# Kernel optimization log

Hardware: AMD Instinct MI355X
Metric: run time of the kernel (lower is better)

## Reference

```python
import jax, jax.numpy as jnp
import numpy as np
import math

N_HEADS = 32
N_REP = 4
N_KV = N_HEADS // N_REP
HEAD_DIM = 128
MAX_SEQ = 4096
BATCH = 8
Q_LEN = 1


def setup_inputs() -> dict:
    key = jax.random.key(0)
    ks = jax.random.split(key, 7)
    input_pos = jax.random.randint(ks[0], (Q_LEN,), 0, MAX_SEQ, dtype=jnp.int32)
    q = jax.random.normal(ks[1], (N_HEADS, BATCH, Q_LEN, HEAD_DIM), dtype=jnp.float32)
    k = jax.random.normal(ks[2], (N_KV, BATCH, Q_LEN, HEAD_DIM), dtype=jnp.float32)
    v = jax.random.normal(ks[3], (N_KV, BATCH, Q_LEN, HEAD_DIM), dtype=jnp.float32)
    k_cache = jax.random.normal(ks[4], (N_KV, BATCH, MAX_SEQ, HEAD_DIM), dtype=jnp.float32)
    v_cache = jax.random.normal(ks[5], (N_KV, BATCH, MAX_SEQ, HEAD_DIM), dtype=jnp.float32)
    mask = jax.random.normal(ks[6], (MAX_SEQ, MAX_SEQ), dtype=jnp.float32)
    return {"input_pos": input_pos, "q": q, "k": k, "v": v,
            "k_cache": k_cache, "v_cache": v_cache, "mask": mask}


def reference(input_pos, q, k, v, k_cache, v_cache, mask):
    # KV cache update (index_put_ at positions input_pos along seq axis)
    kc = k_cache.at[:, :, input_pos, :].set(k)   # [G, B, S, D]
    vc = v_cache.at[:, :, input_pos, :].set(v)   # [G, B, S, D]
    scale = 1.0 / math.sqrt(HEAD_DIM)
    # group query heads by kv head: head i uses kv group i // n_rep
    qg = q.reshape(N_KV, N_REP, BATCH, Q_LEN, HEAD_DIM)
    scores = jnp.einsum('grbqd,gbsd->grbqs', qg, kc) * scale
    scores = scores + mask[input_pos]            # [Q, S] broadcast
    probs = jax.nn.softmax(scores, axis=-1)
    out = jnp.einsum('grbqs,gbsd->grbqd', probs, vc)  # [G, R, B, Q, D]
    # torch.cat over heads (i = g*n_rep + r) on last dim -> [B, Q, H*D]
    out = out.transpose(2, 3, 0, 1, 4).reshape(BATCH, Q_LEN, N_HEADS * HEAD_DIM)
    return out
```

## Files before the change

### kernel.cpp

```cpp
#include <hip/hip_runtime.h>
#include <math.h>

#define NKV    8
#define NREP   4
#define NH     32
#define BATCH  8
#define D      128
#define SEQ    4096
#define CHUNKS 16
#define CS     256
#define PSTRIDE 130

__global__ __launch_bounds__(256, 4) void attn_partial(
    const int*   __restrict__ input_pos,
    const float* __restrict__ q,
    const float* __restrict__ knew,
    const float* __restrict__ vnew,
    const float* __restrict__ kcache,
    const float* __restrict__ vcache,
    const float* __restrict__ mask,
    float*       __restrict__ ws)
{
    const int pair = blockIdx.x;
    const int c    = blockIdx.y;
    const int g    = pair >> 3;
    const int b    = pair & 7;
    const int t    = threadIdx.x;
    const int w    = t >> 6;
    const int lane = t & 63;
    const int p4   = lane >> 4;
    const int l16  = lane & 15;
    const int half = lane >> 5;
    const int l32  = lane & 31;
    const int pos  = input_pos[0];

    __shared__ float sc[NREP][CS];
    __shared__ float ml[NREP][2];
    __shared__ float opart[4][NREP][D];

    const float  scale  = 0.08838834764831845f;
    const size_t kvbase = (size_t)(g * BATCH + b) * SEQ * D;
    const float* kbase  = kcache + kvbase;
    const float* vbase  = vcache + kvbase;
    const float* mrow   = mask + (size_t)pos * SEQ;
    const float* knewr  = knew + (size_t)(g * BATCH + b) * D;
    const float* vnewr  = vnew + (size_t)(g * BATCH + b) * D;
    const int    s0     = c * CS;
    const int    rowbase = w * 64;

    float4 qv[NREP][2];
    #pragma unroll
    for (int r = 0; r < NREP; ++r) {
        const float4* qr = (const float4*)(q + ((size_t)(g * NREP + r) * BATCH + b) * D
                                           + l16 * 8);
        qv[r][0] = qr[0];
        qv[r][1] = qr[1];
    }

    #pragma unroll
    for (int i = 0; i < 16; ++i) {
        const int sl = rowbase + i * 4 + p4;
        const int s  = s0 + sl;
        const float* krow = (s == pos) ? knewr : (kbase + (size_t)s * D);
        const float4* k4  = (const float4*)(krow + l16 * 8);
        const float4 k0 = k4[0], k1 = k4[1];
        float acc[NREP];
        #pragma unroll
        for (int r = 0; r < NREP; ++r) {
            float a;
            a = k0.x * qv[r][0].x;
            a = fmaf(k0.y, qv[r][0].y, a);
            a = fmaf(k0.z, qv[r][0].z, a);
            a = fmaf(k0.w, qv[r][0].w, a);
            a = fmaf(k1.x, qv[r][1].x, a);
            a = fmaf(k1.y, qv[r][1].y, a);
            a = fmaf(k1.z, qv[r][1].z, a);
            a = fmaf(k1.w, qv[r][1].w, a);
            acc[r] = a;
        }
        #pragma unroll
        for (int off = 1; off < 16; off <<= 1) {
            #pragma unroll
            for (int r = 0; r < NREP; ++r)
                acc[r] += __shfl_xor(acc[r], off);
        }
        if (l16 == 0) {
            const float mval = mrow[s];
            #pragma unroll
            for (int r = 0; r < NREP; ++r)
                sc[r][sl] = fmaf(acc[r], scale, mval);
        }
    }
    __syncthreads();

    {
        const int r = w;
        float v0 = sc[r][lane];
        float v1 = sc[r][lane + 64];
        float v2 = sc[r][lane + 128];
        float v3 = sc[r][lane + 192];
        float m  = fmaxf(fmaxf(v0, v1), fmaxf(v2, v3));
        #pragma unroll
        for (int off = 1; off < 64; off <<= 1)
            m = fmaxf(m, __shfl_xor(m, off));
        float e0 = __expf(v0 - m);
        float e1 = __expf(v1 - m);
        float e2 = __expf(v2 - m);
        float e3 = __expf(v3 - m);
        sc[r][lane]       = e0;
        sc[r][lane + 64]  = e1;
        sc[r][lane + 128] = e2;
        sc[r][lane + 192] = e3;
        float l = (e0 + e1) + (e2 + e3);
        #pragma unroll
        for (int off = 1; off < 64; off <<= 1)
            l += __shfl_xor(l, off);
        if (lane == 0) { ml[r][0] = m; ml[r][1] = l; }
    }
    __syncthreads();

    float4 oacc[NREP];
    #pragma unroll
    for (int r = 0; r < NREP; ++r) oacc[r] = make_float4(0.f, 0.f, 0.f, 0.f);

    #pragma unroll
    for (int it = 0; it < 32; ++it) {
        const int sl = rowbase + it * 2 + half;
        const int s  = s0 + sl;
        const float* vrow = (s == pos) ? vnewr : (vbase + (size_t)s * D);
        const float4 v4 = *(const float4*)(vrow + l32 * 4);
        #pragma unroll
        for (int r = 0; r < NREP; ++r) {
            const float pr = sc[r][sl];
            oacc[r].x = fmaf(pr, v4.x, oacc[r].x);
            oacc[r].y = fmaf(pr, v4.y, oacc[r].y);
            oacc[r].z = fmaf(pr, v4.z, oacc[r].z);
            oacc[r].w = fmaf(pr, v4.w, oacc[r].w);
        }
    }
    #pragma unroll
    for (int r = 0; r < NREP; ++r) {
        oacc[r].x += __shfl_xor(oacc[r].x, 32);
        oacc[r].y += __shfl_xor(oacc[r].y, 32);
        oacc[r].z += __shfl_xor(oacc[r].z, 32);
        oacc[r].w += __shfl_xor(oacc[r].w, 32);
    }
    if (half == 0) {
        #pragma unroll
        for (int r = 0; r < NREP; ++r)
            *(float4*)&opart[w][r][l32 * 4] = oacc[r];
    }
    __syncthreads();

    #pragma unroll
    for (int ii = 0; ii < 2; ++ii) {
        int idx = t + ii * 256;
        int r   = idx >> 7;
        int d   = idx & 127;
        float sum = opart[0][r][d] + opart[1][r][d]
                  + opart[2][r][d] + opart[3][r][d];
        size_t base = (((size_t)pair * CHUNKS + c) * NREP + r) * PSTRIDE;
        ws[base + d] = sum;
        if (d == 0) { ws[base + 128] = ml[r][0]; ws[base + 129] = ml[r][1]; }
    }
}

__global__ __launch_bounds__(128) void attn_reduce(
    const float* __restrict__ ws, float* __restrict__ out)
{
    const int idx  = blockIdx.x;
    const int pair = idx >> 2;
    const int r    = idx & 3;
    const int g    = pair >> 3;
    const int b    = pair & 7;
    const int d    = threadIdx.x;

    float mv[CHUNKS], lv[CHUNKS];
    float M = -INFINITY;
    #pragma unroll
    for (int c = 0; c < CHUNKS; ++c) {
        size_t base = (((size_t)pair * CHUNKS + c) * NREP + r) * PSTRIDE;
        float2 t = *(const float2*)&ws[base + 128];
        mv[c] = t.x; lv[c] = t.y;
        M = fmaxf(M, t.x);
    }
    float acc = 0.f, L = 0.f;
    #pragma unroll
    for (int c = 0; c < CHUNKS; ++c) {
        size_t base = (((size_t)pair * CHUNKS + c) * NREP + r) * PSTRIDE;
        float wgt = __expf(mv[c] - M);
        acc += ws[base + d] * wgt;
        L   += lv[c] * wgt;
    }
    int h = g * NREP + r;
    out[(size_t)b * (NH * D) + h * D + d] = acc / L;
}

__global__ __launch_bounds__(256) void attn_full(
    const int*   __restrict__ input_pos,
    const float* __restrict__ q,
    const float* __restrict__ knew,
    const float* __restrict__ vnew,
    const float* __restrict__ kcache,
    const float* __restrict__ vcache,
    const float* __restrict__ mask,
    float*       __restrict__ out)
{
    const int idx = blockIdx.x;
    const int h   = idx >> 3;
    const int b   = idx & 7;
    const int g   = h >> 2;
    const int t   = threadIdx.x;
    const int wave = t >> 6, lane = t & 63, half = lane >> 5, l32 = lane & 31;
    const int pos = input_pos[0];

    __shared__ float sc[SEQ];
    __shared__ float wred[4];
    __shared__ float oacc[2][D];

    const size_t kvbase = (size_t)(g * BATCH + b) * SEQ * D;
    const float* kbase  = kcache + kvbase;
    const float* vbase  = vcache + kvbase;
    const float* mrow   = mask + (size_t)pos * SEQ;
    const float* knewr  = knew + (size_t)(g * BATCH + b) * D;
    const float* vnewr  = vnew + (size_t)(g * BATCH + b) * D;
    const float  scale  = 0.08838834764831845f;

    float4 qv = ((const float4*)(q + (size_t)(h * BATCH + b) * D))[l32];

    for (int p = 0; p < SEQ / 8; ++p) {
        int s = p * 8 + wave * 2 + half;
        const float4* krow = (s == pos) ? (const float4*)knewr
                                        : (const float4*)(kbase + (size_t)s * D);
        float4 kv = krow[l32];
        float acc = qv.x * kv.x + qv.y * kv.y + qv.z * kv.z + qv.w * kv.w;
        #pragma unroll
        for (int off = 1; off < 32; off <<= 1)
            acc += __shfl_xor(acc, off);
        if (l32 == 0) sc[s] = acc * scale + mrow[s];
    }
    __syncthreads();

    float m = -INFINITY;
    for (int s = t; s < SEQ; s += 256) m = fmaxf(m, sc[s]);
    #pragma unroll
    for (int off = 1; off < 64; off <<= 1) m = fmaxf(m, __shfl_xor(m, off));
    if (lane == 0) wred[wave] = m;
    __syncthreads();
    m = fmaxf(fmaxf(wred[0], wred[1]), fmaxf(wred[2], wred[3]));
    __syncthreads();

    float l = 0.f;
    for (int s = t; s < SEQ; s += 256) { float e = __expf(sc[s] - m); sc[s] = e; l += e; }
    #pragma unroll
    for (int off = 1; off < 64; off <<= 1) l += __shfl_xor(l, off);
    __syncthreads();
    if (lane == 0) wred[wave] = l;
    __syncthreads();
    float L = wred[0] + wred[1] + wred[2] + wred[3];

    {
        int hf = t >> 7, d = t & 127;
        float acc = 0.f;
        for (int s = hf * (SEQ / 2); s < (hf + 1) * (SEQ / 2); ++s) {
            const float* vrow = (s == pos) ? vnewr : (vbase + (size_t)s * D);
            acc += sc[s] * vrow[d];
        }
        oacc[hf][d] = acc;
    }
    __syncthreads();
    if (t < D) out[(size_t)b * (NH * D) + h * D + t] = (oacc[0][t] + oacc[1][t]) / L;
}

extern "C" void kernel_launch(void* const* d_in, const int* in_sizes, int n_in,
                              void* d_out, int out_size, void* d_ws, size_t ws_size,
                              hipStream_t stream) {
    const int*   input_pos = (const int*)  d_in[0];
    const float* q         = (const float*)d_in[1];
    const float* k         = (const float*)d_in[2];
    const float* v         = (const float*)d_in[3];
    const float* kcache    = (const float*)d_in[4];
    const float* vcache    = (const float*)d_in[5];
    const float* mask      = (const float*)d_in[6];
    float* out = (float*)d_out;

    const size_t need = (size_t)64 * CHUNKS * NREP * PSTRIDE * sizeof(float);
    if (ws_size >= need) {
        dim3 g1(64, CHUNKS);
        attn_partial<<<g1, 256, 0, stream>>>(input_pos, q, k, v, kcache, vcache, mask,
                                             (float*)d_ws);
        attn_reduce<<<256, 128, 0, stream>>>((const float*)d_ws, out);
    } else {
        attn_full<<<256, 256, 0, stream>>>(input_pos, q, k, v, kcache, vcache, mask, out);
    }
}
```

Before: 54.56 us.

## Make each wavefront an independent 64-row split to drop block barriers

Each wavefront now owns its own 64-position strip and computes its own softmax max and sum. It writes its partial output and statistics straight to the workspace, which removes all three __syncthreads and the cross-wave shared-memory reduction. In exchange the workspace holds four times as many partials (64 strips instead of 16 chunks). The reduce kernel now loops over a runtime chunk count without unrolling, so it reads more data and may stall more on loads.

```diff
diff --git a/kernel.cpp b/kernel.cpp
--- a/kernel.cpp
+++ b/kernel.cpp
@@ -7,8 +7,7 @@
 #define BATCH  8
 #define D      128
 #define SEQ    4096
-#define CHUNKS 16
-#define CS     256
+#define STRIPS 64
 #define PSTRIDE 130
 
 __global__ __launch_bounds__(256, 4) void attn_partial(
@@ -22,7 +21,6 @@
     float*       __restrict__ ws)
 {
     const int pair = blockIdx.x;
-    const int c    = blockIdx.y;
     const int g    = pair >> 3;
     const int b    = pair & 7;
     const int t    = threadIdx.x;
@@ -33,10 +31,11 @@
     const int half = lane >> 5;
     const int l32  = lane & 31;
     const int pos  = input_pos[0];
-
-    __shared__ float sc[NREP][CS];
-    __shared__ float ml[NREP][2];
-    __shared__ float opart[4][NREP][D];
+    const int strip = blockIdx.y * 4 + w;
+    const int s0    = strip * 64;
+
+    __shared__ float sc_all[4][NREP][STRIPS];
+    float (*scw)[STRIPS] = sc_all[w];
 
     const float  scale  = 0.08838834764831845f;
     const size_t kvbase = (size_t)(g * BATCH + b) * SEQ * D;
@@ -45,8 +44,6 @@
     const float* mrow   = mask + (size_t)pos * SEQ;
     const float* knewr  = knew + (size_t)(g * BATCH + b) * D;
     const float* vnewr  = vnew + (size_t)(g * BATCH + b) * D;
-    const int    s0     = c * CS;
-    const int    rowbase = w * 64;
 
     float4 qv[NREP][2];
     #pragma unroll
@@ -59,7 +56,7 @@
 
     #pragma unroll
     for (int i = 0; i < 16; ++i) {
-        const int sl = rowbase + i * 4 + p4;
+        const int sl = i * 4 + p4;
         const int s  = s0 + sl;
         const float* krow = (s == pos) ? knewr : (kbase + (size_t)s * D);
         const float4* k4  = (const float4*)(krow + l16 * 8);
@@ -88,36 +85,36 @@
             const float mval = mrow[s];
             #pragma unroll
             for (int r = 0; r < NREP; ++r)
-                sc[r][sl] = fmaf(acc[r], scale, mval);
-        }
-    }
-    __syncthreads();
-
+                scw[r][sl] = fmaf(acc[r], scale, mval);
+        }
+    }
+
+    const int rep  = lane >> 4;
+    const int row0 = lane & 15;
+    float mO, lO;
     {
-        const int r = w;
-        float v0 = sc[r][lane];
-        float v1 = sc[r][lane + 64];
-        float v2 = sc[r][lane + 128];
-        float v3 = sc[r][lane + 192];
+        float v0 = scw[rep][row0];
+        float v1 = scw[rep][row0 + 16];
+        float v2 = scw[rep][row0 + 32];
+        float v3 = scw[rep][row0 + 48];
         float m  = fmaxf(fmaxf(v0, v1), fmaxf(v2, v3));
         #pragma unroll
-        for (int off = 1; off < 64; off <<= 1)
+        for (int off = 1; off < 16; off <<= 1)
             m = fmaxf(m, __shfl_xor(m, off));
         float e0 = __expf(v0 - m);
         float e1 = __expf(v1 - m);
         float e2 = __expf(v2 - m);
         float e3 = __expf(v3 - m);
-        sc[r][lane]       = e0;
-        sc[r][lane + 64]  = e1;
-        sc[r][lane + 128] = e2;
-        sc[r][lane + 192] = e3;
+        scw[rep][row0]      = e0;
+        scw[rep][row0 + 16] = e1;
+        scw[rep][row0 + 32] = e2;
+        scw[rep][row0 + 48] = e3;
         float l = (e0 + e1) + (e2 + e3);
         #pragma unroll
-        for (int off = 1; off < 64; off <<= 1)
+        for (int off = 1; off < 16; off <<= 1)
             l += __shfl_xor(l, off);
-        if (lane == 0) { ml[r][0] = m; ml[r][1] = l; }
-    }
-    __syncthreads();
+        mO = m; lO = l;
+    }
 
     float4 oacc[NREP];
     #pragma unroll
@@ -125,13 +122,13 @@
 
     #pragma unroll
     for (int it = 0; it < 32; ++it) {
-        const int sl = rowbase + it * 2 + half;
+        const int sl = it * 2 + half;
         const int s  = s0 + sl;
         const float* vrow = (s == pos) ? vnewr : (vbase + (size_t)s * D);
         const float4 v4 = *(const float4*)(vrow + l32 * 4);
         #pragma unroll
         for (int r = 0; r < NREP; ++r) {
-            const float pr = sc[r][sl];
+            const float pr = scw[r][sl];
             oacc[r].x = fmaf(pr, v4.x, oacc[r].x);
             oacc[r].y = fmaf(pr, v4.y, oacc[r].y);
             oacc[r].z = fmaf(pr, v4.z, oacc[r].z);
@@ -145,28 +142,21 @@
         oacc[r].z += __shfl_xor(oacc[r].z, 32);
         oacc[r].w += __shfl_xor(oacc[r].w, 32);
     }
+
+    const size_t base0 = (((size_t)pair * STRIPS + strip) * NREP) * PSTRIDE;
     if (half == 0) {
         #pragma unroll
         for (int r = 0; r < NREP; ++r)
-            *(float4*)&opart[w][r][l32 * 4] = oacc[r];
-    }
-    __syncthreads();
-
-    #pragma unroll
-    for (int ii = 0; ii < 2; ++ii) {
-        int idx = t + ii * 256;
-        int r   = idx >> 7;
-        int d   = idx & 127;
-        float sum = opart[0][r][d] + opart[1][r][d]
-                  + opart[2][r][d] + opart[3][r][d];
-        size_t base = (((size_t)pair * CHUNKS + c) * NREP + r) * PSTRIDE;
-        ws[base + d] = sum;
-        if (d == 0) { ws[base + 128] = ml[r][0]; ws[base + 129] = ml[r][1]; }
+            *(float4*)&ws[base0 + (size_t)r * PSTRIDE + l32 * 4] = oacc[r];
+    }
+    if (row0 == 0) {
+        ws[base0 + (size_t)rep * PSTRIDE + 128] = mO;
+        ws[base0 + (size_t)rep * PSTRIDE + 129] = lO;
     }
 }
 
 __global__ __launch_bounds__(128) void attn_reduce(
-    const float* __restrict__ ws, float* __restrict__ out)
+    const float* __restrict__ ws, float* __restrict__ out, int nchunks)
 {
     const int idx  = blockIdx.x;
     const int pair = idx >> 2;
@@ -175,22 +165,18 @@
     const int b    = pair & 7;
     const int d    = threadIdx.x;
 
-    float mv[CHUNKS], lv[CHUNKS];
+    const size_t base0 = (((size_t)pair * nchunks) * NREP + r) * PSTRIDE;
+    const size_t cstep = (size_t)NREP * PSTRIDE;
+
     float M = -INFINITY;
-    #pragma unroll
-    for (int c = 0; c < CHUNKS; ++c) {
-        size_t base = (((size_t)pair * CHUNKS + c) * NREP + r) * PSTRIDE;
-        float2 t = *(const float2*)&ws[base + 128];
-        mv[c] = t.x; lv[c] = t.y;
-        M = fmaxf(M, t.x);
-    }
+    for (int c = 0; c < nchunks; ++c)
+        M = fmaxf(M, ws[base0 + c * cstep + 128]);
     float acc = 0.f, L = 0.f;
-    #pragma unroll
-    for (int c = 0; c < CHUNKS; ++c) {
-        size_t base = (((size_t)pair * CHUNKS + c) * NREP + r) * PSTRIDE;
-        float wgt = __expf(mv[c] - M);
+    for (int c = 0; c < nchunks; ++c) {
+        size_t base = base0 + c * cstep;
+        float wgt = __expf(ws[base + 128] - M);
         acc += ws[base + d] * wgt;
-        L   += lv[c] * wgt;
+        L   += ws[base + 129] * wgt;
     }
     int h = g * NREP + r;
     out[(size_t)b * (NH * D) + h * D + d] = acc / L;
@@ -284,12 +270,12 @@
     const float* mask      = (const float*)d_in[6];
     float* out = (float*)d_out;
 
-    const size_t need = (size_t)64 * CHUNKS * NREP * PSTRIDE * sizeof(float);
+    const size_t need = (size_t)64 * STRIPS * NREP * PSTRIDE * sizeof(float);
     if (ws_size >= need) {
-        dim3 g1(64, CHUNKS);
+        dim3 g1(64, 16);
         attn_partial<<<g1, 256, 0, stream>>>(input_pos, q, k, v, kcache, vcache, mask,
                                              (float*)d_ws);
-        attn_reduce<<<256, 128, 0, stream>>>((const float*)d_ws, out);
+        attn_reduce<<<256, 128, 0, stream>>>((const float*)d_ws, out, STRIPS);
     } else {
         attn_full<<<256, 256, 0, stream>>>(input_pos, q, k, v, kcache, vcache, mask, out);
     }
```

Result: slower. 79.02 us (+44.8%).
